# Optimization experiments

Hardware: AMD Instinct MI355X
Metric: run time of the kernel (lower is better)

## Reference

```python
import jax, jax.numpy as jnp
import numpy as np

IMG = 128; P = 16; ND = IMG // P; N = ND * ND  # 64 patches
INF = 3 * P * P      # 768 flattened patch features
ATT = 768; HID = 3072; OUT = 768; B = 64
EPS = 1e-5


def setup_inputs() -> dict:
    key = jax.random.key(0)
    ks = jax.random.split(key, 24)
    w = lambda k, shape: jax.random.normal(k, shape, jnp.float32) * 0.02
    return {
        "x": jax.random.normal(ks[0], (B, 3, IMG, IMG), jnp.float32),
        # per-patch q/k/v projections: [n, in, out] weights, [n, out] biases
        "Wq": w(ks[1], (N, INF, ATT)), "bq": w(ks[2], (N, ATT)),
        "Wk": w(ks[3], (N, INF, ATT)), "bk": w(ks[4], (N, ATT)),
        "Wv": w(ks[5], (N, INF, ATT)), "bv": w(ks[6], (N, ATT)),
        "ln_g": jnp.ones((ATT,), jnp.float32), "ln_b": jnp.zeros((ATT,), jnp.float32),
        "p1_w": w(ks[7], (INF, ATT)), "p1_b": w(ks[8], (ATT,)),
        "w0": w(ks[9], (ATT, HID)),  "b0": w(ks[10], (HID,)),
        "w1": w(ks[11], (HID, HID)), "b1": w(ks[12], (HID,)),
        "w2": w(ks[13], (HID, HID)), "b2": w(ks[14], (HID,)),
        "w3": w(ks[15], (HID, HID)), "b3": w(ks[16], (HID,)),
        "w4": w(ks[17], (HID, OUT)), "b4": w(ks[18], (OUT,)),
        "p2_w": w(ks[19], (ATT, OUT)), "p2_b": w(ks[20], (OUT,)),
    }


def _forward(x, Wq, bq, Wk, bk, Wv, bv, ln_g, ln_b, p1_w, p1_b,
             w0, b0, w1, b1, w2, b2, w3, b3, w4, b4, p2_w, p2_b):
    b_ = x.shape[0]
    # patch split (row-major over (i,j) blocks) then flatten channel*patch dims
    flat = x.reshape(b_, 3, ND, P, ND, P).transpose(0, 2, 4, 1, 3, 5).reshape(b_, N, INF)
    # per-patch projections, attention taken ACROSS the batch dim (as in source)
    q = jnp.einsum('bnf,nfd->bnd', flat, Wq) + bq
    k = jnp.einsum('bnf,nfd->bnd', flat, Wk) + bk
    v = jnp.einsum('bnf,nfd->bnd', flat, Wv) + bv
    scores = jnp.einsum('bnd,cnd->nbc', q, k) / jnp.sqrt(jnp.float32(ATT))  # [n,B,B]
    attn = jnp.einsum('nbc,cnd->bnd', jax.nn.softmax(scores, axis=-1), v)  # [B,n,ATT]
    # LayerNorm(att_features)
    mu = attn.mean(-1, keepdims=True)
    var = ((attn - mu) ** 2).mean(-1, keepdims=True)
    ln = (attn - mu) / jnp.sqrt(var + EPS) * ln_g + ln_b
    att = ln + flat @ p1_w + p1_b
    # linear stack (no nonlinearity in the source)
    h = att @ w0 + b0
    h = h @ w1 + b1
    h = h @ w2 + b2
    h = h @ w3 + b3
    h = h @ w4 + b4
    proj = h + att @ p2_w + p2_b
    return jax.nn.softmax(proj, axis=2)


def reference(x, Wq, bq, Wk, bk, Wv, bv, ln_g, ln_b, p1_w, p1_b,
              w0, b0, w1, b1, w2, b2, w3, b3, w4, b4, p2_w, p2_b):
    return _forward(x, Wq, bq, Wk, bk, Wv, bv, ln_g, ln_b, p1_w, p1_b,
                    w0, b0, w1, b1, w2, b2, w3, b3, w4, b4, p2_w, p2_b)
```

## Files before the change

kernel.cpp:

```cpp
#include <hip/hip_runtime.h>
#include <hip/hip_bf16.h>

using bf16 = __bf16;
using bf16x4 = __bf16 __attribute__((ext_vector_type(4)));
using bf16x8 = __bf16 __attribute__((ext_vector_type(8)));
using f32x4 = float __attribute__((ext_vector_type(4)));

static constexpr long ROWEL = 64L * 768;

__device__ __forceinline__ void async16(void* lds, const void* g)
{
    __builtin_amdgcn_global_load_lds((const __attribute__((address_space(1))) void*)g,
                                     (__attribute__((address_space(3))) void*)lds, 16, 0, 0);
}

__global__ __launch_bounds__(256) void k_patchify(const float* __restrict__ x, bf16* __restrict__ flat)
{
    const int n = blockIdx.x;
    const int b = blockIdx.y;
    const int i_ = n >> 3, j_ = n & 7;
    for (int it = 0; it < 3; ++it) {
        int f = threadIdx.x + it * 256;
        int c = f >> 8, rem = f & 255, pi = rem >> 4, pj = rem & 15;
        float v = x[(((long)(b * 3 + c)) << 14) + ((i_ * 16 + pi) << 7) + (j_ * 16 + pj)];
        flat[(long)b * ROWEL + n * 768 + f] = (bf16)v;
    }
}

__global__ __launch_bounds__(256) void k_cvt_t2(
    const float* __restrict__ W0, bf16* __restrict__ T0,
    const float* __restrict__ W1, bf16* __restrict__ T1)
{
    const int z = blockIdx.z;
    const float* W = z ? W1 : W0;
    bf16* Wt = z ? T1 : T0;
    const int Kd = z ? 768 : 3072, Nd = 768;
    if (z && blockIdx.x >= 12) return;
    __shared__ bf16 T[64 * 66];
    const int k0 = blockIdx.x * 64, n0 = blockIdx.y * 64;
    const int tid = threadIdx.x;
    const int kr = tid >> 4, nc = (tid & 15) * 4;
#pragma unroll
    for (int i = 0; i < 4; ++i) {
        f32x4 v = *(const f32x4*)(W + (long)(k0 + kr + i * 16) * Nd + n0 + nc);
#pragma unroll
        for (int e = 0; e < 4; ++e)
            T[(kr + i * 16) * 66 + nc + e] = (bf16)v[e];
    }
    __syncthreads();
    const int nr = tid >> 3, ks = (tid & 7) * 8;
#pragma unroll
    for (int it = 0; it < 2; ++it) {
        int n = nr + it * 32;
        bf16x8 o;
#pragma unroll
        for (int j = 0; j < 8; ++j) o[j] = T[(ks + j) * 66 + n];
        *(bf16x8*)(Wt + (long)(n0 + n) * Kd + k0 + ks) = o;
    }
}

__global__ __launch_bounds__(256) void k_cast4(
    const float* __restrict__ s0, bf16* __restrict__ d0,
    const float* __restrict__ s1, bf16* __restrict__ d1,
    const float* __restrict__ s2, bf16* __restrict__ d2,
    const float* __restrict__ s3, bf16* __restrict__ d3)
{
    const int z = blockIdx.y;
    const float* W = z == 0 ? s0 : z == 1 ? s1 : z == 2 ? s2 : s3;
    bf16* o = z == 0 ? d0 : z == 1 ? d1 : z == 2 ? d2 : d3;
    const long nelem = z == 0 ? 768L * 3072 : 3072L * 3072;
    long i = ((long)blockIdx.x * 256 + threadIdx.x) * 8;
    if (i >= nelem) return;
    f32x4 a = *(const f32x4*)(W + i);
    f32x4 b = *(const f32x4*)(W + i + 4);
    bf16x8 v;
#pragma unroll
    for (int e = 0; e < 4; ++e) { v[e] = (bf16)a[e]; v[4 + e] = (bf16)b[e]; }
    *(bf16x8*)(o + i) = v;
}

template<int BM, int BN>
__global__ __launch_bounds__(256) void k_gemm_bt(
    const bf16* __restrict__ A, long lda,
    const bf16* __restrict__ Bt, long ldb,
    int K,
    const float* __restrict__ bias,
    const float* __restrict__ addm,
    bf16* __restrict__ Cb, float* __restrict__ Cf, long ldc)
{
    constexpr int WM = BM / 2, WN = BN / 2, FM = WM / 16, FN = WN / 16;
    __shared__ bf16 As[2][BM * 32];
    __shared__ bf16 Bs[2][BN * 32];
    const int tid = threadIdx.x, lane = tid & 63, wave = tid >> 6;
    const int wm = wave >> 1, wn = wave & 1;
    const long m0 = (long)blockIdx.x * BM, n0 = (long)blockIdx.y * BN;

    f32x4 acc[FM][FN];
#pragma unroll
    for (int i = 0; i < FM; ++i)
#pragma unroll
        for (int j = 0; j < FN; ++j) acc[i][j] = (f32x4){0.f, 0.f, 0.f, 0.f};

    const int nk = K >> 5;

    auto stage = [&](int buf, int kt) {
        const long kb = (long)kt * 32;
#pragma unroll
        for (int i = 0; i < BM / 64; ++i) {
            const int c = i * 256 + tid;
            const int r = c >> 2, seg = c & 3;
            async16(&As[buf][(i * 256 + wave * 64) * 8], A + (m0 + r) * lda + kb + seg * 8);
        }
#pragma unroll
        for (int i = 0; i < BN / 64; ++i) {
            const int c = i * 256 + tid;
            const int r = c >> 2, seg = c & 3;
            async16(&Bs[buf][(i * 256 + wave * 64) * 8], Bt + (n0 + r) * ldb + kb + seg * 8);
        }
    };

    stage(0, 0);
    __syncthreads();
    int cur = 0;
    for (int kt = 0; kt < nk; ++kt) {
        if (kt + 1 < nk) stage(cur ^ 1, kt + 1);
        bf16x8 af[FM], bfr[FN];
#pragma unroll
        for (int i = 0; i < FM; ++i)
            af[i] = *(const bf16x8*)&As[cur][(wm * WM + i * 16 + (lane & 15)) * 32 + (lane >> 4) * 8];
#pragma unroll
        for (int j = 0; j < FN; ++j)
            bfr[j] = *(const bf16x8*)&Bs[cur][(wn * WN + j * 16 + (lane & 15)) * 32 + (lane >> 4) * 8];
#pragma unroll
        for (int i = 0; i < FM; ++i)
#pragma unroll
            for (int j = 0; j < FN; ++j)
                acc[i][j] = __builtin_amdgcn_mfma_f32_16x16x32_bf16(af[i], bfr[j], acc[i][j], 0, 0, 0);
        __syncthreads();
        cur ^= 1;
    }

#pragma unroll
    for (int j = 0; j < FN; ++j) {
        const long col = n0 + wn * WN + j * 16 + (lane & 15);
        const float bb = bias ? bias[col] : 0.f;
#pragma unroll
        for (int i = 0; i < FM; ++i) {
#pragma unroll
            for (int r = 0; r < 4; ++r) {
                const long row = m0 + wm * WM + i * 16 + (lane >> 4) * 4 + r;
                const long idx = row * ldc + col;
                float v = acc[i][j][r] + bb;
                if (addm) v += addm[idx];
                if (Cb) Cb[idx] = (bf16)v;
                if (Cf) Cf[idx] = v;
            }
        }
    }
}

template<int BM, int BN>
__global__ __launch_bounds__(256) void k_gemm_btsk(
    const bf16* __restrict__ A, long lda,
    const bf16* __restrict__ Bt, long ldb,
    int Ks,
    float* __restrict__ Cp, long zstride, long ldc)
{
    constexpr int WM = BM / 2, WN = BN / 2, FM = WM / 16, FN = WN / 16;
    __shared__ bf16 As[2][BM * 32];
    __shared__ bf16 Bs[2][BN * 32];
    const int tid = threadIdx.x, lane = tid & 63, wave = tid >> 6;
    const int wm = wave >> 1, wn = wave & 1;
    const long m0 = (long)blockIdx.x * BM, n0 = (long)blockIdx.y * BN;
    const long kofs = (long)blockIdx.z * Ks;

    f32x4 acc[FM][FN];
#pragma unroll
    for (int i = 0; i < FM; ++i)
#pragma unroll
        for (int j = 0; j < FN; ++j) acc[i][j] = (f32x4){0.f, 0.f, 0.f, 0.f};

    const int nk = Ks >> 5;

    auto stage = [&](int buf, int kt) {
        const long kb = kofs + (long)kt * 32;
#pragma unroll
        for (int i = 0; i < BM / 64; ++i) {
            const int c = i * 256 + tid;
            const int r = c >> 2, seg = c & 3;
            async16(&As[buf][(i * 256 + wave * 64) * 8], A + (m0 + r) * lda + kb + seg * 8);
        }
#pragma unroll
        for (int i = 0; i < BN / 64; ++i) {
            const int c = i * 256 + tid;
            const int r = c >> 2, seg = c & 3;
            async16(&Bs[buf][(i * 256 + wave * 64) * 8], Bt + (n0 + r) * ldb + kb + seg * 8);
        }
    };

    stage(0, 0);
    __syncthreads();
    int cur = 0;
    for (int kt = 0; kt < nk; ++kt) {
        if (kt + 1 < nk) stage(cur ^ 1, kt + 1);
        bf16x8 af[FM], bfr[FN];
#pragma unroll
        for (int i = 0; i < FM; ++i)
            af[i] = *(const bf16x8*)&As[cur][(wm * WM + i * 16 + (lane & 15)) * 32 + (lane >> 4) * 8];
#pragma unroll
        for (int j = 0; j < FN; ++j)
            bfr[j] = *(const bf16x8*)&Bs[cur][(wn * WN + j * 16 + (lane & 15)) * 32 + (lane >> 4) * 8];
#pragma unroll
        for (int i = 0; i < FM; ++i)
#pragma unroll
            for (int j = 0; j < FN; ++j)
                acc[i][j] = __builtin_amdgcn_mfma_f32_16x16x32_bf16(af[i], bfr[j], acc[i][j], 0, 0, 0);
        __syncthreads();
        cur ^= 1;
    }

    float* Cz = Cp + (long)blockIdx.z * zstride;
#pragma unroll
    for (int j = 0; j < FN; ++j) {
        const long col = n0 + wn * WN + j * 16 + (lane & 15);
#pragma unroll
        for (int i = 0; i < FM; ++i)
#pragma unroll
            for (int r = 0; r < 4; ++r) {
                const long row = m0 + wm * WM + i * 16 + (lane >> 4) * 4 + r;
                Cz[row * ldc + col] = acc[i][j][r];
            }
    }
}

__global__ __launch_bounds__(256) void k_skadd(
    const float* __restrict__ P, long zstride, int S, long nelem, bf16* __restrict__ out)
{
    long i = ((long)blockIdx.x * 256 + threadIdx.x) * 4;
    if (i >= nelem) return;
    f32x4 s = *(const f32x4*)(P + i);
    for (int z = 1; z < S; ++z) {
        f32x4 p = *(const f32x4*)(P + (long)z * zstride + i);
        s += p;
    }
    bf16x4 o;
#pragma unroll
    for (int e = 0; e < 4; ++e) o[e] = (bf16)s[e];
    *(bf16x4*)(out + i) = o;
}

__global__ __launch_bounds__(256) void k_skaddT(
    const float* __restrict__ P, long zstride, int S,
    const float* __restrict__ p2w, bf16* __restrict__ Mt)
{
    const int n = blockIdx.x;
    for (int k = threadIdx.x; k < 768; k += 256) {
        float s = p2w[(long)k * 768 + n];
        for (int z = 0; z < S; ++z) s += P[(long)z * zstride + n * 768 + k];
        Mt[n * 768 + k] = (bf16)s;
    }
}

__global__ __launch_bounds__(256) void k_qkv(
    const bf16* __restrict__ flat,
    const float* __restrict__ Wq, const float* __restrict__ Wk, const float* __restrict__ Wv,
    const float* __restrict__ bq, const float* __restrict__ bk, const float* __restrict__ bv,
    bf16* __restrict__ qo, bf16* __restrict__ ko, bf16* __restrict__ vo)
{
    const int zz = blockIdx.z;
    const float* W = zz == 0 ? Wq : zz == 1 ? Wk : Wv;
    const float* bias = zz == 0 ? bq : zz == 1 ? bk : bv;
    bf16* out = zz == 0 ? qo : zz == 1 ? ko : vo;

    __shared__ bf16 As[2][64 * 32];
    __shared__ float Bs[2][32 * 64];
    const int tid = threadIdx.x, lane = tid & 63, wave = tid >> 6;
    const int wm = wave >> 1, wn = wave & 1;
    const int n0 = blockIdx.x * 64;
    const int z = blockIdx.y;
    const float* Wz = W + (long)z * 589824;

    f32x4 acc[2][2];
#pragma unroll
    for (int i = 0; i < 2; ++i)
#pragma unroll
        for (int j = 0; j < 2; ++j) acc[i][j] = (f32x4){0.f, 0.f, 0.f, 0.f};

    auto stage = [&](int buf, int kt) {
        const int kb = kt * 32;
        {
            const int r = tid >> 2, seg = tid & 3;
            async16(&As[buf][wave * 512], flat + (long)r * ROWEL + z * 768 + kb + seg * 8);
        }
#pragma unroll
        for (int i = 0; i < 2; ++i) {
            const int c = i * 256 + tid;
            const int kl = c >> 4, nn = (c & 15) * 4;
            async16(&Bs[buf][(i * 256 + wave * 64) * 4], Wz + (long)(kb + kl) * 768 + n0 + nn);
        }
    };

    stage(0, 0);
    __syncthreads();
    int cur = 0;
    for (int kt = 0; kt < 24; ++kt) {
        if (kt + 1 < 24) stage(cur ^ 1, kt + 1);
        bf16x8 af[2], bfr[2];
#pragma unroll
        for (int i = 0; i < 2; ++i)
            af[i] = *(const bf16x8*)&As[cur][(wm * 32 + i * 16 + (lane & 15)) * 32 + (lane >> 4) * 8];
#pragma unroll
        for (int j = 0; j < 2; ++j) {
            const int n = wn * 32 + j * 16 + (lane & 15);
            const int kf = (lane >> 4) * 8;
            bf16x8 b;
#pragma unroll
            for (int e = 0; e < 8; ++e) b[e] = (bf16)Bs[cur][(kf + e) * 64 + n];
            bfr[j] = b;
        }
#pragma unroll
        for (int i = 0; i < 2; ++i)
#pragma unroll
            for (int j = 0; j < 2; ++j)
                acc[i][j] = __builtin_amdgcn_mfma_f32_16x16x32_bf16(af[i], bfr[j], acc[i][j], 0, 0, 0);
        __syncthreads();
        cur ^= 1;
    }

#pragma unroll
    for (int j = 0; j < 2; ++j) {
        const int col = n0 + wn * 32 + j * 16 + (lane & 15);
        const float bb = bias[z * 768 + col];
#pragma unroll
        for (int i = 0; i < 2; ++i) {
#pragma unroll
            for (int r = 0; r < 4; ++r) {
                const int row = wm * 32 + i * 16 + (lane >> 4) * 4 + r;
                out[(long)row * ROWEL + z * 768 + col] = (bf16)(acc[i][j][r] + bb);
            }
        }
    }
}

template<typename TW>
__global__ __launch_bounds__(256) void k_vm2(
    const float* __restrict__ Pin, const float* __restrict__ bin, const TW* __restrict__ W,
    int K, int N, float* __restrict__ Pout)
{
    __shared__ float red[4][64];
    const int tid = threadIdx.x;
    const int nl = tid & 63, kq = tid >> 6;
    const int n = blockIdx.x * 64 + nl;
    const int kc = blockIdx.y;
    const int kchunk = K / 8, kslice = kchunk / 4;
    const int k0 = kc * kchunk + kq * kslice;
    float acc = 0.f;
#pragma unroll 4
    for (int k = k0; k < k0 + kslice; ++k) {
        float vk = bin[k];
        if (Pin) {
#pragma unroll
            for (int j = 0; j < 8; ++j) vk += Pin[(long)j * K + k];
        }
        acc += vk * (float)W[(long)k * N + n];
    }
    red[kq][nl] = acc;
    __syncthreads();
    if (kq == 0)
        Pout[(long)kc * N + n] = red[0][nl] + red[1][nl] + red[2][nl] + red[3][nl];
}

__global__ __launch_bounds__(256) void k_vred(
    const float* __restrict__ P, const float* __restrict__ b1, const float* __restrict__ b2,
    int N, float* __restrict__ out)
{
    const int n = blockIdx.x * 256 + threadIdx.x;
    if (n >= N) return;
    float s = b1[n] + (b2 ? b2[n] : 0.f);
#pragma unroll
    for (int j = 0; j < 8; ++j) s += P[(long)j * N + n];
    out[n] = s;
}

__global__ __launch_bounds__(256) void k_attn(
    const bf16* __restrict__ q, const bf16* __restrict__ k, const bf16* __restrict__ v,
    float* __restrict__ attn)
{
    const int n = blockIdx.x;
    __shared__ bf16 QT[64 * 72];
    __shared__ bf16 KT[64 * 72];
    __shared__ float S[64 * 66];
    __shared__ bf16 P[64 * 72];
    __shared__ bf16 VT[128 * 72];

    const int tid = threadIdx.x, lane = tid & 63, wave = tid >> 6;
    const int wm = wave >> 1, wn = wave & 1;

    f32x4 accs[2][2];
#pragma unroll
    for (int i = 0; i < 2; ++i)
#pragma unroll
        for (int j = 0; j < 2; ++j) accs[i][j] = (f32x4){0.f, 0.f, 0.f, 0.f};

    for (int kt = 0; kt < 12; ++kt) {
#pragma unroll
        for (int i = 0; i < 2; ++i) {
            int cid = tid + i * 256;
            int r = cid >> 3, seg = cid & 7;
            *(bf16x8*)&QT[r * 72 + seg * 8] = *(const bf16x8*)(q + (long)r * ROWEL + n * 768 + kt * 64 + seg * 8);
            *(bf16x8*)&KT[r * 72 + seg * 8] = *(const bf16x8*)(k + (long)r * ROWEL + n * 768 + kt * 64 + seg * 8);
        }
        __syncthreads();
#pragma unroll
        for (int ks = 0; ks < 2; ++ks) {
            bf16x8 qa[2], kb[2];
#pragma unroll
            for (int i = 0; i < 2; ++i)
                qa[i] = *(const bf16x8*)&QT[(wm * 32 + i * 16 + (lane & 15)) * 72 + ks * 32 + (lane >> 4) * 8];
#pragma unroll
            for (int j = 0; j < 2; ++j)
                kb[j] = *(const bf16x8*)&KT[(wn * 32 + j * 16 + (lane & 15)) * 72 + ks * 32 + (lane >> 4) * 8];
#pragma unroll
            for (int i = 0; i < 2; ++i)
#pragma unroll
                for (int j = 0; j < 2; ++j)
                    accs[i][j] = __builtin_amdgcn_mfma_f32_16x16x32_bf16(qa[i], kb[j], accs[i][j], 0, 0, 0);
        }
        __syncthreads();
    }
    const float sc = 0.03608439182435161f;
#pragma unroll
    for (int i = 0; i < 2; ++i)
#pragma unroll
        for (int j = 0; j < 2; ++j)
#pragma unroll
            for (int r = 0; r < 4; ++r)
                S[(wm * 32 + i * 16 + (lane >> 4) * 4 + r) * 66 + wn * 32 + j * 16 + (lane & 15)] = accs[i][j][r] * sc;
    __syncthreads();

    {
        int r = tid >> 2, l4 = tid & 3;
        float m = -1e30f;
        for (int c = l4; c < 64; c += 4) m = fmaxf(m, S[r * 66 + c]);
        m = fmaxf(m, __shfl_xor(m, 1));
        m = fmaxf(m, __shfl_xor(m, 2));
        float s = 0.f;
        for (int c = l4; c < 64; c += 4) { float e = __expf(S[r * 66 + c] - m); S[r * 66 + c] = e; s += e; }
        s += __shfl_xor(s, 1);
        s += __shfl_xor(s, 2);
        float inv = 1.f / s;
        for (int c = l4; c < 64; c += 4) P[r * 72 + c] = (bf16)(S[r * 66 + c] * inv);
    }
    __syncthreads();

    for (int dc = 0; dc < 6; ++dc) {
#pragma unroll
        for (int i = 0; i < 4; ++i) {
            int cid = tid + i * 256;
            int c = cid >> 4, seg = cid & 15;
            bf16x8 vv = *(const bf16x8*)(v + (long)c * ROWEL + n * 768 + dc * 128 + seg * 8);
#pragma unroll
            for (int e = 0; e < 8; ++e)
                VT[(seg * 8 + e) * 72 + c] = vv[e];
        }
        __syncthreads();
        f32x4 acco[2][4];
#pragma unroll
        for (int i = 0; i < 2; ++i)
#pragma unroll
            for (int j = 0; j < 4; ++j) acco[i][j] = (f32x4){0.f, 0.f, 0.f, 0.f};
#pragma unroll
        for (int ks = 0; ks < 2; ++ks) {
            bf16x8 pa[2], vb[4];
#pragma unroll
            for (int i = 0; i < 2; ++i)
                pa[i] = *(const bf16x8*)&P[(wm * 32 + i * 16 + (lane & 15)) * 72 + ks * 32 + (lane >> 4) * 8];
#pragma unroll
            for (int j = 0; j < 4; ++j)
                vb[j] = *(const bf16x8*)&VT[(wn * 64 + j * 16 + (lane & 15)) * 72 + ks * 32 + (lane >> 4) * 8];
#pragma unroll
            for (int i = 0; i < 2; ++i)
#pragma unroll
                for (int j = 0; j < 4; ++j)
                    acco[i][j] = __builtin_amdgcn_mfma_f32_16x16x32_bf16(pa[i], vb[j], acco[i][j], 0, 0, 0);
        }
#pragma unroll
        for (int i = 0; i < 2; ++i)
#pragma unroll
            for (int j = 0; j < 4; ++j)
#pragma unroll
                for (int r = 0; r < 4; ++r) {
                    long b = wm * 32 + i * 16 + (lane >> 4) * 4 + r;
                    int d = dc * 128 + wn * 64 + j * 16 + (lane & 15);
                    attn[b * ROWEL + n * 768 + d] = acco[i][j][r];
                }
        __syncthreads();
    }
}

__global__ __launch_bounds__(256) void k_ln(float* __restrict__ a,
                                            const float* __restrict__ g, const float* __restrict__ bb)
{
    const long row = blockIdx.x * 4 + (threadIdx.x >> 6);
    const int lane = threadIdx.x & 63;
    float* p = a + row * 768;
    f32x4 xv[3];
    float s = 0.f;
#pragma unroll
    for (int c = 0; c < 3; ++c) {
        xv[c] = *(const f32x4*)(p + c * 256 + lane * 4);
        s += xv[c][0] + xv[c][1] + xv[c][2] + xv[c][3];
    }
#pragma unroll
    for (int o = 1; o < 64; o <<= 1) s += __shfl_xor(s, o);
    const float mu = s * (1.f / 768.f);
    float vs = 0.f;
#pragma unroll
    for (int c = 0; c < 3; ++c)
#pragma unroll
        for (int e = 0; e < 4; ++e) { float d = xv[c][e] - mu; vs += d * d; }
#pragma unroll
    for (int o = 1; o < 64; o <<= 1) vs += __shfl_xor(vs, o);
    const float rstd = rsqrtf(vs * (1.f / 768.f) + 1e-5f);
#pragma unroll
    for (int c = 0; c < 3; ++c)
#pragma unroll
        for (int e = 0; e < 4; ++e) {
            int col = c * 256 + lane * 4 + e;
            p[col] = (xv[c][e] - mu) * rstd * g[col] + bb[col];
        }
}

__global__ __launch_bounds__(256) void k_softmax(float* __restrict__ o)
{
    const long row = blockIdx.x * 4 + (threadIdx.x >> 6);
    const int lane = threadIdx.x & 63;
    float* p = o + row * 768;
    f32x4 xv[3];
    float m = -1e30f;
#pragma unroll
    for (int c = 0; c < 3; ++c) {
        xv[c] = *(const f32x4*)(p + c * 256 + lane * 4);
        m = fmaxf(m, fmaxf(fmaxf(xv[c][0], xv[c][1]), fmaxf(xv[c][2], xv[c][3])));
    }
#pragma unroll
    for (int o2 = 1; o2 < 64; o2 <<= 1) m = fmaxf(m, __shfl_xor(m, o2));
    float s = 0.f;
#pragma unroll
    for (int c = 0; c < 3; ++c)
#pragma unroll
        for (int e = 0; e < 4; ++e) { float ev = __expf(xv[c][e] - m); xv[c][e] = ev; s += ev; }
#pragma unroll
    for (int o2 = 1; o2 < 64; o2 <<= 1) s += __shfl_xor(s, o2);
    const float inv = 1.f / s;
#pragma unroll
    for (int c = 0; c < 3; ++c)
        *(f32x4*)(p + c * 256 + lane * 4) = xv[c] * inv;
}

extern "C" void kernel_launch(void* const* d_in, const int* in_sizes, int n_in,
                              void* d_out, int out_size, void* d_ws, size_t ws_size,
                              hipStream_t stream)
{
    const float* x   = (const float*)d_in[0];
    const float* Wq  = (const float*)d_in[1];
    const float* bq  = (const float*)d_in[2];
    const float* Wk  = (const float*)d_in[3];
    const float* bk  = (const float*)d_in[4];
    const float* Wv  = (const float*)d_in[5];
    const float* bv  = (const float*)d_in[6];
    const float* lng = (const float*)d_in[7];
    const float* lnb = (const float*)d_in[8];
    const float* p1w = (const float*)d_in[9];
    const float* p1b = (const float*)d_in[10];
    const float* w0  = (const float*)d_in[11];
    const float* b0  = (const float*)d_in[12];
    const float* w1  = (const float*)d_in[13];
    const float* b1  = (const float*)d_in[14];
    const float* w2  = (const float*)d_in[15];
    const float* b2  = (const float*)d_in[16];
    const float* w3  = (const float*)d_in[17];
    const float* b3  = (const float*)d_in[18];
    const float* w4  = (const float*)d_in[19];
    const float* b4  = (const float*)d_in[20];
    const float* p2w = (const float*)d_in[21];
    const float* p2b = (const float*)d_in[22];
    float* out = (float*)d_out;

    char* wsbase = (char*)d_ws;
    size_t off = 0;
    auto alloc = [&](size_t bytes) { char* p = wsbase + off; off += (bytes + 255) & ~(size_t)255; return p; };
    bf16*  flat = (bf16*)alloc(4096L * 768 * 2);
    bf16*  qb   = (bf16*)alloc(4096L * 768 * 2);
    bf16*  kb   = (bf16*)alloc(4096L * 768 * 2);
    bf16*  vb2  = (bf16*)alloc(4096L * 768 * 2);
    float* attn = (float*)alloc(4096L * 768 * 4);
    bf16*  att  = (bf16*)alloc(4096L * 768 * 2);
    bf16*  p1t  = (bf16*)alloc(768L * 768 * 2);
    bf16*  w4t  = (bf16*)alloc(768L * 3072 * 2);
    bf16*  w0c  = (bf16*)alloc(768L * 3072 * 2);
    bf16*  w1c  = (bf16*)alloc(3072L * 3072 * 2);
    bf16*  w2c  = (bf16*)alloc(3072L * 3072 * 2);
    bf16*  w3c  = (bf16*)alloc(3072L * 3072 * 2);
    bf16*  M1   = (bf16*)alloc(768L * 3072 * 2);
    bf16*  M2   = (bf16*)alloc(768L * 3072 * 2);
    bf16*  M3   = (bf16*)alloc(768L * 3072 * 2);
    bf16*  Mt   = (bf16*)alloc(768L * 768 * 2);
    float* Cp   = (float*)alloc(3L * 768 * 3072 * 4);
    float* vPa  = (float*)alloc(8L * 3072 * 4);
    float* vPb  = (float*)alloc(8L * 3072 * 4);
    float* c4   = (float*)alloc(768 * 4);
    if (off > ws_size) return;

    const long ZS = 768L * 3072;
    const long ZS4 = 768L * 768;

    k_patchify<<<dim3(64, 64), 256, 0, stream>>>(x, flat);
    k_cast4<<<dim3(4608, 4), 256, 0, stream>>>(w0, w0c, w1, w1c, w2, w2c, w3, w3c);
    k_cvt_t2<<<dim3(48, 12, 2), 256, 0, stream>>>(w4, w4t, p1w, p1t);

    k_qkv<<<dim3(12, 64, 3), 256, 0, stream>>>(flat, Wq, Wk, Wv, bq, bk, bv, qb, kb, vb2);

    k_attn<<<64, 256, 0, stream>>>(qb, kb, vb2, attn);
    k_ln<<<1024, 256, 0, stream>>>(attn, lng, lnb);
    k_gemm_bt<64, 64><<<dim3(64, 12), 256, 0, stream>>>(flat, 768, p1t, 768, 768, p1b, attn, att, nullptr, 768);

    k_gemm_btsk<64, 64><<<dim3(12, 48, 3), 256, 0, stream>>>(w4t, 3072, w3c, 3072, 1024, Cp, ZS, 3072);
    k_skadd<<<2304, 256, 0, stream>>>(Cp, ZS, 3, ZS, M1);
    k_gemm_btsk<64, 64><<<dim3(12, 48, 3), 256, 0, stream>>>(M1, 3072, w2c, 3072, 1024, Cp, ZS, 3072);
    k_skadd<<<2304, 256, 0, stream>>>(Cp, ZS, 3, ZS, M2);
    k_gemm_btsk<64, 64><<<dim3(12, 48, 3), 256, 0, stream>>>(M2, 3072, w1c, 3072, 1024, Cp, ZS, 3072);
    k_skadd<<<2304, 256, 0, stream>>>(Cp, ZS, 3, ZS, M3);
    k_gemm_btsk<64, 64><<<dim3(12, 12, 6), 256, 0, stream>>>(M3, 3072, w0c, 3072, 512, Cp, ZS4, 768);
    k_skaddT<<<768, 256, 0, stream>>>(Cp, ZS4, 6, p2w, Mt);

    k_vm2<bf16><<<dim3(48, 8), 256, 0, stream>>>(nullptr, b0, w1c, 3072, 3072, vPa);
    k_vm2<bf16><<<dim3(48, 8), 256, 0, stream>>>(vPa, b1, w2c, 3072, 3072, vPb);
    k_vm2<bf16><<<dim3(48, 8), 256, 0, stream>>>(vPb, b2, w3c, 3072, 3072, vPa);
    k_vm2<float><<<dim3(12, 8), 256, 0, stream>>>(vPa, b3, w4, 3072, 768, vPb);
    k_vred<<<3, 256, 0, stream>>>(vPb, b4, p2b, 768, c4);

    k_gemm_bt<64, 64><<<dim3(64, 12), 256, 0, stream>>>(att, 768, Mt, 768, 768, c4, nullptr, nullptr, out, 768);
    k_softmax<<<1024, 256, 0, stream>>>(out);
}
```

Baseline: 570.1 us.

## Replace async LDS loads with register-staged double buffering and split attention grid

Every GEMM now loads tiles into registers, writes them to LDS, and runs MFMA with a two-deep register prefetch, replacing the global_load_lds async path. The two GEMM variants are merged into one kernel with an optional split-K partial-output path. The QKV kernel converts fp32 weights to bf16 during the LDS write rather than during fragment reads. The attention kernel's six-chunk output loop becomes a second grid dimension for more parallelism, at the cost of recomputing the scores and softmax in each block. The change costs extra registers and repeated score work, and the Cp buffer allocation is doubled.

```diff
diff --git a/kernel.cpp b/kernel.cpp
--- a/kernel.cpp
+++ b/kernel.cpp
@@ -7,12 +7,6 @@
 using f32x4 = float __attribute__((ext_vector_type(4)));
 
 static constexpr long ROWEL = 64L * 768;
-
-__device__ __forceinline__ void async16(void* lds, const void* g)
-{
-    __builtin_amdgcn_global_load_lds((const __attribute__((address_space(1))) void*)g,
-                                     (__attribute__((address_space(3))) void*)lds, 16, 0, 0);
-}
 
 __global__ __launch_bounds__(256) void k_patchify(const float* __restrict__ x, bf16* __restrict__ flat)
 {
@@ -79,21 +73,31 @@
     *(bf16x8*)(o + i) = v;
 }
 
+__device__ __forceinline__ void barrier_lgkm()
+{
+    asm volatile("s_waitcnt lgkmcnt(0)" ::: "memory");
+    __builtin_amdgcn_s_barrier();
+    __builtin_amdgcn_sched_barrier(0);
+}
+
 template<int BM, int BN>
-__global__ __launch_bounds__(256) void k_gemm_bt(
+__global__ __launch_bounds__(256) void k_gemm_rs(
     const bf16* __restrict__ A, long lda,
     const bf16* __restrict__ Bt, long ldb,
-    int K,
+    int Ks,
     const float* __restrict__ bias,
     const float* __restrict__ addm,
-    bf16* __restrict__ Cb, float* __restrict__ Cf, long ldc)
+    bf16* __restrict__ Cb, float* __restrict__ Cf, long ldc,
+    float* __restrict__ Cp, long zstride)
 {
     constexpr int WM = BM / 2, WN = BN / 2, FM = WM / 16, FN = WN / 16;
+    constexpr int NA = BM / 64, NB = BN / 64;
     __shared__ bf16 As[2][BM * 32];
     __shared__ bf16 Bs[2][BN * 32];
     const int tid = threadIdx.x, lane = tid & 63, wave = tid >> 6;
     const int wm = wave >> 1, wn = wave & 1;
     const long m0 = (long)blockIdx.x * BM, n0 = (long)blockIdx.y * BN;
+    const long kofs = (long)blockIdx.z * Ks;
 
     f32x4 acc[FM][FN];
 #pragma unroll
@@ -101,45 +105,77 @@
 #pragma unroll
         for (int j = 0; j < FN; ++j) acc[i][j] = (f32x4){0.f, 0.f, 0.f, 0.f};
 
-    const int nk = K >> 5;
-
-    auto stage = [&](int buf, int kt) {
-        const long kb = (long)kt * 32;
-#pragma unroll
-        for (int i = 0; i < BM / 64; ++i) {
-            const int c = i * 256 + tid;
-            const int r = c >> 2, seg = c & 3;
-            async16(&As[buf][(i * 256 + wave * 64) * 8], A + (m0 + r) * lda + kb + seg * 8);
-        }
-#pragma unroll
-        for (int i = 0; i < BN / 64; ++i) {
-            const int c = i * 256 + tid;
-            const int r = c >> 2, seg = c & 3;
-            async16(&Bs[buf][(i * 256 + wave * 64) * 8], Bt + (n0 + r) * ldb + kb + seg * 8);
+    const int nk = Ks >> 5;
+    bf16x8 Xa[NA], Xb[NB], Ya[NA], Yb[NB];
+
+    auto LOAD = [&](bf16x8 (&ra)[NA], bf16x8 (&rb)[NB], int kt) {
+        const long kb = kofs + (long)kt * 32;
+#pragma unroll
+        for (int i = 0; i < NA; ++i) {
+            const int c = i * 256 + tid, r = c >> 2, sg = c & 3;
+            ra[i] = *(const bf16x8*)(A + (m0 + r) * lda + kb + sg * 8);
+        }
+#pragma unroll
+        for (int i = 0; i < NB; ++i) {
+            const int c = i * 256 + tid, r = c >> 2, sg = c & 3;
+            rb[i] = *(const bf16x8*)(Bt + (n0 + r) * ldb + kb + sg * 8);
         }
     };
-
-    stage(0, 0);
-    __syncthreads();
-    int cur = 0;
-    for (int kt = 0; kt < nk; ++kt) {
-        if (kt + 1 < nk) stage(cur ^ 1, kt + 1);
+    auto WRITE = [&](bf16x8 (&ra)[NA], bf16x8 (&rb)[NB], int buf) {
+#pragma unroll
+        for (int i = 0; i < NA; ++i)
+            *(bf16x8*)&As[buf][(i * 256 + tid) * 8] = ra[i];
+#pragma unroll
+        for (int i = 0; i < NB; ++i)
+            *(bf16x8*)&Bs[buf][(i * 256 + tid) * 8] = rb[i];
+    };
+    auto COMPUTE = [&](int buf) {
         bf16x8 af[FM], bfr[FN];
 #pragma unroll
         for (int i = 0; i < FM; ++i)
-            af[i] = *(const bf16x8*)&As[cur][(wm * WM + i * 16 + (lane & 15)) * 32 + (lane >> 4) * 8];
+            af[i] = *(const bf16x8*)&As[buf][(wm * WM + i * 16 + (lane & 15)) * 32 + (lane >> 4) * 8];
 #pragma unroll
         for (int j = 0; j < FN; ++j)
-            bfr[j] = *(const bf16x8*)&Bs[cur][(wn * WN + j * 16 + (lane & 15)) * 32 + (lane >> 4) * 8];
+            bfr[j] = *(const bf16x8*)&Bs[buf][(wn * WN + j * 16 + (lane & 15)) * 32 + (lane >> 4) * 8];
 #pragma unroll
         for (int i = 0; i < FM; ++i)
 #pragma unroll
             for (int j = 0; j < FN; ++j)
                 acc[i][j] = __builtin_amdgcn_mfma_f32_16x16x32_bf16(af[i], bfr[j], acc[i][j], 0, 0, 0);
-        __syncthreads();
-        cur ^= 1;
-    }
-
+    };
+
+    LOAD(Xa, Xb, 0);
+    LOAD(Ya, Yb, 1);
+    WRITE(Xa, Xb, 0);
+    barrier_lgkm();
+    for (int t = 0; t < nk; t += 2) {
+        if (t + 2 < nk) LOAD(Xa, Xb, t + 2);
+        COMPUTE(0);
+        if (t + 1 < nk) WRITE(Ya, Yb, 1);
+        barrier_lgkm();
+        if (t + 1 < nk) {
+            if (t + 3 < nk) LOAD(Ya, Yb, t + 3);
+            COMPUTE(1);
+            if (t + 2 < nk) WRITE(Xa, Xb, 0);
+            barrier_lgkm();
+        }
+    }
+
+    if (Cp) {
+        float* Cz = Cp + (long)blockIdx.z * zstride;
+#pragma unroll
+        for (int j = 0; j < FN; ++j) {
+            const long col = n0 + wn * WN + j * 16 + (lane & 15);
+#pragma unroll
+            for (int i = 0; i < FM; ++i)
+#pragma unroll
+                for (int r = 0; r < 4; ++r) {
+                    const long row = m0 + wm * WM + i * 16 + (lane >> 4) * 4 + r;
+                    Cz[row * ldc + col] = acc[i][j][r];
+                }
+        }
+        return;
+    }
 #pragma unroll
     for (int j = 0; j < FN; ++j) {
         const long col = n0 + wn * WN + j * 16 + (lane & 15);
@@ -159,77 +195,96 @@
     }
 }
 
-template<int BM, int BN>
-__global__ __launch_bounds__(256) void k_gemm_btsk(
-    const bf16* __restrict__ A, long lda,
-    const bf16* __restrict__ Bt, long ldb,
-    int Ks,
-    float* __restrict__ Cp, long zstride, long ldc)
-{
-    constexpr int WM = BM / 2, WN = BN / 2, FM = WM / 16, FN = WN / 16;
-    __shared__ bf16 As[2][BM * 32];
-    __shared__ bf16 Bs[2][BN * 32];
+__global__ __launch_bounds__(256) void k_qkv(
+    const bf16* __restrict__ flat,
+    const float* __restrict__ Wq, const float* __restrict__ Wk, const float* __restrict__ Wv,
+    const float* __restrict__ bq, const float* __restrict__ bk, const float* __restrict__ bv,
+    bf16* __restrict__ qo, bf16* __restrict__ ko, bf16* __restrict__ vo)
+{
+    const int zz = blockIdx.z;
+    const float* W = zz == 0 ? Wq : zz == 1 ? Wk : Wv;
+    const float* bias = zz == 0 ? bq : zz == 1 ? bk : bv;
+    bf16* out = zz == 0 ? qo : zz == 1 ? ko : vo;
+
+    __shared__ bf16 As[2][64 * 32];
+    __shared__ bf16 Bs[2][64 * 32];
     const int tid = threadIdx.x, lane = tid & 63, wave = tid >> 6;
     const int wm = wave >> 1, wn = wave & 1;
-    const long m0 = (long)blockIdx.x * BM, n0 = (long)blockIdx.y * BN;
-    const long kofs = (long)blockIdx.z * Ks;
-
-    f32x4 acc[FM][FN];
-#pragma unroll
-    for (int i = 0; i < FM; ++i)
-#pragma unroll
-        for (int j = 0; j < FN; ++j) acc[i][j] = (f32x4){0.f, 0.f, 0.f, 0.f};
-
-    const int nk = Ks >> 5;
-
-    auto stage = [&](int buf, int kt) {
-        const long kb = kofs + (long)kt * 32;
-#pragma unroll
-        for (int i = 0; i < BM / 64; ++i) {
-            const int c = i * 256 + tid;
-            const int r = c >> 2, seg = c & 3;
-            async16(&As[buf][(i * 256 + wave * 64) * 8], A + (m0 + r) * lda + kb + seg * 8);
-        }
-#pragma unroll
-        for (int i = 0; i < BN / 64; ++i) {
-            const int c = i * 256 + tid;
-            const int r = c >> 2, seg = c & 3;
-            async16(&Bs[buf][(i * 256 + wave * 64) * 8], Bt + (n0 + r) * ldb + kb + seg * 8);
-        }
+    const int n0 = blockIdx.x * 64;
+    const int z = blockIdx.y;
+    const float* Wz = W + (long)z * 589824;
+
+    f32x4 acc[2][2];
+#pragma unroll
+    for (int i = 0; i < 2; ++i)
+#pragma unroll
+        for (int j = 0; j < 2; ++j) acc[i][j] = (f32x4){0.f, 0.f, 0.f, 0.f};
+
+    const int bcol = tid & 63;
+    const int bkg = (tid >> 6) * 8;
+    bf16x8 Xa, Ya;
+    float Xb[8], Yb[8];
+
+    auto LOAD = [&](bf16x8& ra, float (&rb)[8], int kt) {
+        const int kb = kt * 32;
+        const int r = tid >> 2, sg = tid & 3;
+        ra = *(const bf16x8*)(flat + (long)r * ROWEL + z * 768 + kb + sg * 8);
+#pragma unroll
+        for (int e = 0; e < 8; ++e)
+            rb[e] = Wz[(long)(kb + bkg + e) * 768 + n0 + bcol];
     };
-
-    stage(0, 0);
-    __syncthreads();
-    int cur = 0;
-    for (int kt = 0; kt < nk; ++kt) {
-        if (kt + 1 < nk) stage(cur ^ 1, kt + 1);
-        bf16x8 af[FM], bfr[FN];
-#pragma unroll
-        for (int i = 0; i < FM; ++i)
-            af[i] = *(const bf16x8*)&As[cur][(wm * WM + i * 16 + (lane & 15)) * 32 + (lane >> 4) * 8];
-#pragma unroll
-        for (int j = 0; j < FN; ++j)
-            bfr[j] = *(const bf16x8*)&Bs[cur][(wn * WN + j * 16 + (lane & 15)) * 32 + (lane >> 4) * 8];
-#pragma unroll
-        for (int i = 0; i < FM; ++i)
-#pragma unroll
-            for (int j = 0; j < FN; ++j)
+    auto WRITE = [&](bf16x8& ra, float (&rb)[8], int buf) {
+        *(bf16x8*)&As[buf][tid * 8] = ra;
+        bf16x8 bb;
+#pragma unroll
+        for (int e = 0; e < 8; ++e) bb[e] = (bf16)rb[e];
+        *(bf16x8*)&Bs[buf][bcol * 32 + bkg] = bb;
+    };
+    auto COMPUTE = [&](int buf) {
+        bf16x8 af[2], bfr[2];
+#pragma unroll
+        for (int i = 0; i < 2; ++i)
+            af[i] = *(const bf16x8*)&As[buf][(wm * 32 + i * 16 + (lane & 15)) * 32 + (lane >> 4) * 8];
+#pragma unroll
+        for (int j = 0; j < 2; ++j)
+            bfr[j] = *(const bf16x8*)&Bs[buf][(wn * 32 + j * 16 + (lane & 15)) * 32 + (lane >> 4) * 8];
+#pragma unroll
+        for (int i = 0; i < 2; ++i)
+#pragma unroll
+            for (int j = 0; j < 2; ++j)
                 acc[i][j] = __builtin_amdgcn_mfma_f32_16x16x32_bf16(af[i], bfr[j], acc[i][j], 0, 0, 0);
-        __syncthreads();
-        cur ^= 1;
-    }
-
-    float* Cz = Cp + (long)blockIdx.z * zstride;
-#pragma unroll
-    for (int j = 0; j < FN; ++j) {
-        const long col = n0 + wn * WN + j * 16 + (lane & 15);
-#pragma unroll
-        for (int i = 0; i < FM; ++i)
+    };
+
+    const int nk = 24;
+    LOAD(Xa, Xb, 0);
+    LOAD(Ya, Yb, 1);
+    WRITE(Xa, Xb, 0);
+    barrier_lgkm();
+    for (int t = 0; t < nk; t += 2) {
+        if (t + 2 < nk) LOAD(Xa, Xb, t + 2);
+        COMPUTE(0);
+        if (t + 1 < nk) WRITE(Ya, Yb, 1);
+        barrier_lgkm();
+        if (t + 1 < nk) {
+            if (t + 3 < nk) LOAD(Ya, Yb, t + 3);
+            COMPUTE(1);
+            if (t + 2 < nk) WRITE(Xa, Xb, 0);
+            barrier_lgkm();
+        }
+    }
+
+#pragma unroll
+    for (int j = 0; j < 2; ++j) {
+        const int col = n0 + wn * 32 + j * 16 + (lane & 15);
+        const float bb = bias[z * 768 + col];
+#pragma unroll
+        for (int i = 0; i < 2; ++i) {
 #pragma unroll
             for (int r = 0; r < 4; ++r) {
-                const long row = m0 + wm * WM + i * 16 + (lane >> 4) * 4 + r;
-                Cz[row * ldc + col] = acc[i][j][r];
+                const int row = wm * 32 + i * 16 + (lane >> 4) * 4 + r;
+                out[(long)row * ROWEL + z * 768 + col] = (bf16)(acc[i][j][r] + bb);
             }
+        }
     }
 }
 
@@ -258,87 +313,6 @@
         float s = p2w[(long)k * 768 + n];
         for (int z = 0; z < S; ++z) s += P[(long)z * zstride + n * 768 + k];
         Mt[n * 768 + k] = (bf16)s;
-    }
-}
-
-__global__ __launch_bounds__(256) void k_qkv(
-    const bf16* __restrict__ flat,
-    const float* __restrict__ Wq, const float* __restrict__ Wk, const float* __restrict__ Wv,
-    const float* __restrict__ bq, const float* __restrict__ bk, const float* __restrict__ bv,
-    bf16* __restrict__ qo, bf16* __restrict__ ko, bf16* __restrict__ vo)
-{
-    const int zz = blockIdx.z;
-    const float* W = zz == 0 ? Wq : zz == 1 ? Wk : Wv;
-    const float* bias = zz == 0 ? bq : zz == 1 ? bk : bv;
-    bf16* out = zz == 0 ? qo : zz == 1 ? ko : vo;
-
-    __shared__ bf16 As[2][64 * 32];
-    __shared__ float Bs[2][32 * 64];
-    const int tid = threadIdx.x, lane = tid & 63, wave = tid >> 6;
-    const int wm = wave >> 1, wn = wave & 1;
-    const int n0 = blockIdx.x * 64;
-    const int z = blockIdx.y;
-    const float* Wz = W + (long)z * 589824;
-
-    f32x4 acc[2][2];
-#pragma unroll
-    for (int i = 0; i < 2; ++i)
-#pragma unroll
-        for (int j = 0; j < 2; ++j) acc[i][j] = (f32x4){0.f, 0.f, 0.f, 0.f};
-
-    auto stage = [&](int buf, int kt) {
-        const int kb = kt * 32;
-        {
-            const int r = tid >> 2, seg = tid & 3;
-            async16(&As[buf][wave * 512], flat + (long)r * ROWEL + z * 768 + kb + seg * 8);
-        }
-#pragma unroll
-        for (int i = 0; i < 2; ++i) {
-            const int c = i * 256 + tid;
-            const int kl = c >> 4, nn = (c & 15) * 4;
-            async16(&Bs[buf][(i * 256 + wave * 64) * 4], Wz + (long)(kb + kl) * 768 + n0 + nn);
-        }
-    };
-
-    stage(0, 0);
-    __syncthreads();
-    int cur = 0;
-    for (int kt = 0; kt < 24; ++kt) {
-        if (kt + 1 < 24) stage(cur ^ 1, kt + 1);
-        bf16x8 af[2], bfr[2];
-#pragma unroll
-        for (int i = 0; i < 2; ++i)
-            af[i] = *(const bf16x8*)&As[cur][(wm * 32 + i * 16 + (lane & 15)) * 32 + (lane >> 4) * 8];
-#pragma unroll
-        for (int j = 0; j < 2; ++j) {
-            const int n = wn * 32 + j * 16 + (lane & 15);
-            const int kf = (lane >> 4) * 8;
-            bf16x8 b;
-#pragma unroll
-            for (int e = 0; e < 8; ++e) b[e] = (bf16)Bs[cur][(kf + e) * 64 + n];
-            bfr[j] = b;
-        }
-#pragma unroll
-        for (int i = 0; i < 2; ++i)
-#pragma unroll
-            for (int j = 0; j < 2; ++j)
-                acc[i][j] = __builtin_amdgcn_mfma_f32_16x16x32_bf16(af[i], bfr[j], acc[i][j], 0, 0, 0);
-        __syncthreads();
-        cur ^= 1;
-    }
-
-#pragma unroll
-    for (int j = 0; j < 2; ++j) {
-        const int col = n0 + wn * 32 + j * 16 + (lane & 15);
-        const float bb = bias[z * 768 + col];
-#pragma unroll
-        for (int i = 0; i < 2; ++i) {
-#pragma unroll
-            for (int r = 0; r < 4; ++r) {
-                const int row = wm * 32 + i * 16 + (lane >> 4) * 4 + r;
-                out[(long)row * ROWEL + z * 768 + col] = (bf16)(acc[i][j][r] + bb);
-            }
-        }
     }
 }
 
@@ -386,7 +360,8 @@
     const bf16* __restrict__ q, const bf16* __restrict__ k, const bf16* __restrict__ v,
     float* __restrict__ attn)
 {
-    const int n = blockIdx.x;
+    const int dc = blockIdx.x;
+    const int n = blockIdx.y;
     __shared__ bf16 QT[64 * 72];
     __shared__ bf16 KT[64 * 72];
     __shared__ float S[64 * 66];
@@ -413,18 +388,18 @@
         __syncthreads();
 #pragma unroll
         for (int ks = 0; ks < 2; ++ks) {
-            bf16x8 qa[2], kb[2];
+            bf16x8 qa[2], kb2[2];
 #pragma unroll
             for (int i = 0; i < 2; ++i)
                 qa[i] = *(const bf16x8*)&QT[(wm * 32 + i * 16 + (lane & 15)) * 72 + ks * 32 + (lane >> 4) * 8];
 #pragma unroll
             for (int j = 0; j < 2; ++j)
-                kb[j] = *(const bf16x8*)&KT[(wn * 32 + j * 16 + (lane & 15)) * 72 + ks * 32 + (lane >> 4) * 8];
+                kb2[j] = *(const bf16x8*)&KT[(wn * 32 + j * 16 + (lane & 15)) * 72 + ks * 32 + (lane >> 4) * 8];
 #pragma unroll
             for (int i = 0; i < 2; ++i)
 #pragma unroll
                 for (int j = 0; j < 2; ++j)
-                    accs[i][j] = __builtin_amdgcn_mfma_f32_16x16x32_bf16(qa[i], kb[j], accs[i][j], 0, 0, 0);
+                    accs[i][j] = __builtin_amdgcn_mfma_f32_16x16x32_bf16(qa[i], kb2[j], accs[i][j], 0, 0, 0);
         }
         __syncthreads();
     }
@@ -453,7 +428,7 @@
     }
     __syncthreads();
 
-    for (int dc = 0; dc < 6; ++dc) {
+    {
 #pragma unroll
         for (int i = 0; i < 4; ++i) {
             int cid = tid + i * 256;
@@ -494,7 +469,6 @@
                     int d = dc * 128 + wn * 64 + j * 16 + (lane & 15);
                     attn[b * ROWEL + n * 768 + d] = acco[i][j][r];
                 }
-        __syncthreads();
     }
 }
 
@@ -606,7 +580,7 @@
     bf16*  M2   = (bf16*)alloc(768L * 3072 * 2);
     bf16*  M3   = (bf16*)alloc(768L * 3072 * 2);
     bf16*  Mt   = (bf16*)alloc(768L * 768 * 2);
-    float* Cp   = (float*)alloc(3L * 768 * 3072 * 4);
+    float* Cp   = (float*)alloc(6L * 768 * 3072 * 4);
     float* vPa  = (float*)alloc(8L * 3072 * 4);
     float* vPb  = (float*)alloc(8L * 3072 * 4);
     float* c4   = (float*)alloc(768 * 4);
@@ -621,17 +595,17 @@
 
     k_qkv<<<dim3(12, 64, 3), 256, 0, stream>>>(flat, Wq, Wk, Wv, bq, bk, bv, qb, kb, vb2);
 
-    k_attn<<<64, 256, 0, stream>>>(qb, kb, vb2, attn);
+    k_attn<<<dim3(6, 64), 256, 0, stream>>>(qb, kb, vb2, attn);
     k_ln<<<1024, 256, 0, stream>>>(attn, lng, lnb);
-    k_gemm_bt<64, 64><<<dim3(64, 12), 256, 0, stream>>>(flat, 768, p1t, 768, 768, p1b, attn, att, nullptr, 768);
-
-    k_gemm_btsk<64, 64><<<dim3(12, 48, 3), 256, 0, stream>>>(w4t, 3072, w3c, 3072, 1024, Cp, ZS, 3072);
+    k_gemm_rs<64, 64><<<dim3(64, 12), 256, 0, stream>>>(flat, 768, p1t, 768, 768, p1b, attn, att, nullptr, 768, nullptr, 0);
+
+    k_gemm_rs<64, 64><<<dim3(12, 48, 3), 256, 0, stream>>>(w4t, 3072, w3c, 3072, 1024, nullptr, nullptr, nullptr, nullptr, 3072, Cp, ZS);
     k_skadd<<<2304, 256, 0, stream>>>(Cp, ZS, 3, ZS, M1);
-    k_gemm_btsk<64, 64><<<dim3(12, 48, 3), 256, 0, stream>>>(M1, 3072, w2c, 3072, 1024, Cp, ZS, 3072);
+    k_gemm_rs<64, 64><<<dim3(12, 48, 3), 256, 0, stream>>>(M1, 3072, w2c, 3072, 1024, nullptr, nullptr, nullptr, nullptr, 3072, Cp, ZS);
     k_skadd<<<2304, 256, 0, stream>>>(Cp, ZS, 3, ZS, M2);
-    k_gemm_btsk<64, 64><<<dim3(12, 48, 3), 256, 0, stream>>>(M2, 3072, w1c, 3072, 1024, Cp, ZS, 3072);
+    k_gemm_rs<64, 64><<<dim3(12, 48, 3), 256, 0, stream>>>(M2, 3072, w1c, 3072, 1024, nullptr, nullptr, nullptr, nullptr, 3072, Cp, ZS);
     k_skadd<<<2304, 256, 0, stream>>>(Cp, ZS, 3, ZS, M3);
-    k_gemm_btsk<64, 64><<<dim3(12, 12, 6), 256, 0, stream>>>(M3, 3072, w0c, 3072, 512, Cp, ZS4, 768);
+    k_gemm_rs<64, 64><<<dim3(12, 12, 6), 256, 0, stream>>>(M3, 3072, w0c, 3072, 512, nullptr, nullptr, nullptr, nullptr, 768, Cp, ZS4);
     k_skaddT<<<768, 256, 0, stream>>>(Cp, ZS4, 6, p2w, Mt);
 
     k_vm2<bf16><<<dim3(48, 8), 256, 0, stream>>>(nullptr, b0, w1c, 3072, 3072, vPa);
@@ -640,6 +614,6 @@
     k_vm2<float><<<dim3(12, 8), 256, 0, stream>>>(vPa, b3, w4, 3072, 768, vPb);
     k_vred<<<3, 256, 0, stream>>>(vPb, b4, p2b, 768, c4);
 
-    k_gemm_bt<64, 64><<<dim3(64, 12), 256, 0, stream>>>(att, 768, Mt, 768, 768, c4, nullptr, nullptr, out, 768);
+    k_gemm_rs<64, 64><<<dim3(64, 12), 256, 0, stream>>>(att, 768, Mt, 768, 768, c4, nullptr, nullptr, out, 768, nullptr, 0);
     k_softmax<<<1024, 256, 0, stream>>>(out);
 }
```

After: 577.5 us. About the same (+1.3%).
